# Kernel tuning notes

Measured on AMD Instinct MI355X. Metric: run time of the kernel, lower is better.

The kernel has to match this reference:

```python
import jax, jax.numpy as jnp
import numpy as np

DIM = 1024
DEPTH = 2
D_STATE = 16
EXPAND = 2            # standard Mamba expand factor -> d_inner = 2*dim
D_CONV = 4
DT_RANK = DIM // 16   # ceil(dim/16) = 64
D_INNER = DIM * EXPAND
BATCH = 2
SEQ = 1024


def setup_inputs() -> dict:
    key = jax.random.key(0)
    ks = jax.random.split(key, 8)
    def n(k, shape, scale):
        return jax.random.normal(k, shape, jnp.float32) * scale
    # A_log initialized as log(1..N) per channel (S4D-real init, as in mamba_ssm)
    A_log = jnp.tile(jnp.log(jnp.arange(1, D_STATE + 1, dtype=jnp.float32))[None, None, :],
                     (DEPTH, D_INNER, 1))
    return {
        "x": n(ks[0], (BATCH, SEQ, DIM), 1.0),
        "in_proj_w": n(ks[1], (DEPTH, 2 * D_INNER, DIM), DIM ** -0.5),
        "conv_w": n(ks[2], (DEPTH, D_INNER, D_CONV), D_CONV ** -0.5),
        "conv_b": jnp.zeros((DEPTH, D_INNER), jnp.float32),
        "x_proj_w": n(ks[3], (DEPTH, DT_RANK + 2 * D_STATE, D_INNER), D_INNER ** -0.5),
        "dt_proj_w": n(ks[4], (DEPTH, D_INNER, DT_RANK), DT_RANK ** -0.5),
        "dt_proj_b": n(ks[5], (DEPTH, D_INNER), 0.1),
        "A_log": A_log,
        "D": jnp.ones((DEPTH, D_INNER), jnp.float32),
        "out_proj_w": n(ks[6], (DEPTH, DIM, D_INNER), D_INNER ** -0.5),
    }


def _mamba_layer(x, in_w, cw, cb, xp_w, dtw, dtb, A_log, Dp, ow):
    # x: [B, L, dim]
    Bsz = x.shape[0]
    xz = jnp.einsum('bld,ed->ble', x, in_w)            # [B, L, 2*d_inner]
    xi, z = jnp.split(xz, 2, axis=-1)
    # causal depthwise conv1d over time
    xc = jnp.transpose(xi, (0, 2, 1))                  # [B, d_inner, L]
    xc = jax.lax.conv_general_dilated(xc, cw[:, None, :], (1,), [(D_CONV - 1, 0)],
                                      feature_group_count=D_INNER)
    xc = xc + cb[None, :, None]
    xc = jax.nn.silu(jnp.transpose(xc, (0, 2, 1)))     # [B, L, d_inner]
    # input-dependent dt, B, C
    x_dbl = jnp.einsum('bld,ed->ble', xc, xp_w)        # [B, L, dt_rank+2*N]
    dt_raw = x_dbl[..., :DT_RANK]
    Bm = x_dbl[..., DT_RANK:DT_RANK + D_STATE]         # [B, L, N]
    Cm = x_dbl[..., DT_RANK + D_STATE:]                # [B, L, N]
    dt = jax.nn.softplus(jnp.einsum('blr,dr->bld', dt_raw, dtw) + dtb)  # [B, L, d_inner]
    A = -jnp.exp(A_log)                                # [d_inner, N]
    dA = jnp.exp(dt[..., None] * A[None, None])        # [B, L, d_inner, N]
    dBu = dt[..., None] * Bm[:, :, None, :] * xc[..., None]

    def step(h, inp):
        dA_t, dBu_t, C_t = inp
        h = dA_t * h + dBu_t                           # [B, d_inner, N]
        y = jnp.einsum('bdn,bn->bd', h, C_t)
        return h, y

    h0 = jnp.zeros((Bsz, D_INNER, D_STATE), x.dtype)
    _, ys = jax.lax.scan(step, h0,
                         (dA.transpose(1, 0, 2, 3), dBu.transpose(1, 0, 2, 3),
                          Cm.transpose(1, 0, 2)))
    y = ys.transpose(1, 0, 2) + Dp[None, None, :] * xc
    y = y * jax.nn.silu(z)
    return jnp.einsum('bld,od->blo', y, ow)


def reference(x, in_proj_w, conv_w, conv_b, x_proj_w, dt_proj_w, dt_proj_b, A_log, D, out_proj_w):
    for i in range(DEPTH):
        x = _mamba_layer(x, in_proj_w[i], conv_w[i], conv_b[i], x_proj_w[i],
                         dt_proj_w[i], dt_proj_b[i], A_log[i], D[i], out_proj_w[i])
    return x
```

## Files before the change

### kernel.cpp

```cpp
#include <hip/hip_runtime.h>
#include <hip/hip_bf16.h>

typedef __hip_bfloat16 bf16;
typedef __attribute__((ext_vector_type(8))) short short8;
typedef __attribute__((ext_vector_type(4))) short shortx4;
typedef __attribute__((ext_vector_type(4))) float floatx4;

#define BATCH   2
#define SEQ     1024
#define DIM     1024
#define D_INNER 2048
#define D_STATE 16
#define DT_RANK 64
#define MROWS   (BATCH * SEQ)
#define CHUNK   32
#define NCHUNK  (SEQ / CHUNK)

__device__ __forceinline__ float bf2f(bf16 x) { return __bfloat162float(x); }
__device__ __forceinline__ bf16  f2bf(float x) { return __float2bfloat16(x); }
__device__ __forceinline__ short bfbits(float x) {
    bf16 b = __float2bfloat16(x); short s; __builtin_memcpy(&s, &b, 2); return s;
}

__device__ __forceinline__ void ld_lds16(const void* g, void* l) {
    __builtin_amdgcn_global_load_lds(
        (const __attribute__((address_space(1))) void*)g,
        (__attribute__((address_space(3))) void*)l, 16, 0, 0);
}

__device__ __forceinline__ void cast4(const float* in, short* o, int i) {
    floatx4 v = ((const floatx4*)in)[i];
    shortx4 r;
    r.x = bfbits(v.x); r.y = bfbits(v.y); r.z = bfbits(v.z); r.w = bfbits(v.w);
    ((shortx4*)o)[i] = r;
}
__global__ __launch_bounds__(256) void cast_k(
    const float* __restrict__ in, short* __restrict__ o, int n4)
{
    int i = blockIdx.x * 256 + threadIdx.x;
    if (i < n4) cast4(in, o, i);
}
__global__ __launch_bounds__(256) void cast2_k(
    const float* __restrict__ a, short* __restrict__ oa, int na4,
    const float* __restrict__ b, short* __restrict__ ob, int nb4)
{
    int i = blockIdx.x * 256 + threadIdx.x;
    if (i < na4) cast4(a, oa, i);
    else if (i - na4 < nb4) cast4(b, ob, i - na4);
}

__device__ __forceinline__ short8 ld8_any(const void* p, size_t eoff, int is_f32) {
    if (is_f32) {
        const float* f = (const float*)p + eoff;
        floatx4 a = *(const floatx4*)f;
        floatx4 b = *(const floatx4*)(f + 4);
        short8 r;
        r[0] = bfbits(a[0]); r[1] = bfbits(a[1]); r[2] = bfbits(a[2]); r[3] = bfbits(a[3]);
        r[4] = bfbits(b[0]); r[5] = bfbits(b[1]); r[6] = bfbits(b[2]); r[7] = bfbits(b[3]);
        return r;
    } else {
        return *(const short8*)((const bf16*)p + eoff);
    }
}

__global__ __launch_bounds__(256) void gemm128(
    const bf16* __restrict__ A, int lda,
    const bf16* __restrict__ B, int ldb,
    float* __restrict__ Cf, bf16* __restrict__ Cb, int ldc,
    int kchunk, size_t psize)
{
    __shared__ short As[4][128 * 32];
    __shared__ short Bs[4][128 * 32];
    const int tid  = threadIdx.x;
    const int wave = tid >> 6;
    const int lane = tid & 63;
    const int m0 = blockIdx.y * 128;
    const int n0 = blockIdx.x * 128;
    const int wm = (wave & 1) * 64;
    const int wn = (wave >> 1) * 64;
    const int r16  = lane & 15;
    const int quad = lane >> 4;
    const int r0   = tid >> 2;
    const int csw   = (((tid & 3) ^ ((r0 >> 1) & 3)) << 3);
    const int swoff = ((quad ^ ((r16 >> 1) & 3)) << 3);
    const int kbeg = blockIdx.z * kchunk;
    const int nk   = kchunk >> 5;

    floatx4 acc[4][4] = {};

    auto STAGE = [&](int buf, int kk) {
        ld_lds16(A + (size_t)(m0 + r0) * lda + kk + csw,      &As[buf][tid * 8]);
        ld_lds16(A + (size_t)(m0 + r0 + 64) * lda + kk + csw, &As[buf][(tid + 256) * 8]);
        ld_lds16(B + (size_t)(n0 + r0) * ldb + kk + csw,      &Bs[buf][tid * 8]);
        ld_lds16(B + (size_t)(n0 + r0 + 64) * ldb + kk + csw, &Bs[buf][(tid + 256) * 8]);
    };
    auto COMPUTE = [&](int buf) {
        const short* Ab = As[buf];
        const short* Bb = Bs[buf];
        short8 af[4], bg[4];
#pragma unroll
        for (int i = 0; i < 4; i++) {
            af[i] = *(const short8*)(Ab + (wm + i * 16 + r16) * 32 + swoff);
            bg[i] = *(const short8*)(Bb + (wn + i * 16 + r16) * 32 + swoff);
        }
        __builtin_amdgcn_s_setprio(1);
#pragma unroll
        for (int i = 0; i < 4; i++)
#pragma unroll
            for (int j = 0; j < 4; j++)
                acc[i][j] = __builtin_amdgcn_mfma_f32_16x16x32_bf16(af[i], bg[j], acc[i][j], 0, 0, 0);
        __builtin_amdgcn_s_setprio(0);
    };

    STAGE(0, kbeg);
    STAGE(1, kbeg + 32);
    int it = 0;
    for (; it < nk - 2; ++it) {
        STAGE((it + 2) & 3, kbeg + (it + 2) * 32);
        asm volatile("s_waitcnt vmcnt(8) lgkmcnt(0)" ::: "memory");
        __builtin_amdgcn_s_barrier();
        __builtin_amdgcn_sched_barrier(0);
        COMPUTE(it & 3);
    }
    asm volatile("s_waitcnt vmcnt(4) lgkmcnt(0)" ::: "memory");
    __builtin_amdgcn_s_barrier();
    __builtin_amdgcn_sched_barrier(0);
    COMPUTE(it & 3);
    ++it;
    asm volatile("s_waitcnt vmcnt(0) lgkmcnt(0)" ::: "memory");
    __builtin_amdgcn_s_barrier();
    __builtin_amdgcn_sched_barrier(0);
    COMPUTE(it & 3);

    float* Cfp = Cf ? Cf + (size_t)blockIdx.z * psize : nullptr;
#pragma unroll
    for (int i = 0; i < 4; i++)
#pragma unroll
        for (int j = 0; j < 4; j++) {
            int gm = m0 + wm + i * 16 + quad * 4;
            int gn = n0 + wn + j * 16 + r16;
#pragma unroll
            for (int r = 0; r < 4; r++) {
                size_t o = (size_t)(gm + r) * ldc + gn;
                float v = acc[i][j][r];
                if (Cfp) Cfp[o] = v;
                if (Cb) Cb[o] = f2bf(v);
            }
        }
}

__global__ __launch_bounds__(256) void gemm_bt(
    const void* __restrict__ A, int a_f32, int lda,
    const void* __restrict__ B, int b_f32, int ldb,
    float* __restrict__ Cf, bf16* __restrict__ Cb, int ldc,
    int N, int K, size_t psize,
    const float* __restrict__ bias, int act)
{
    __shared__ short As[64][40];
    __shared__ short Bs[64][40];
    const int m0   = blockIdx.y * 64;
    const int n0   = blockIdx.x * 64;
    const int tid  = threadIdx.x;
    const int wave = tid >> 6;
    const int lane = tid & 63;
    const int srow = tid >> 2;
    const int scol = (tid & 3) << 3;
    const int r16  = lane & 15;
    const int quad = lane >> 4;
    const int kbeg = blockIdx.z * K;

    floatx4 acc[4] = {};

    for (int k0 = kbeg; k0 < kbeg + K; k0 += 32) {
        short8 av = ld8_any(A, (size_t)(m0 + srow) * lda + k0 + scol, a_f32);
        short8 bv = {};
        int gn = n0 + srow;
        if (gn < N) bv = ld8_any(B, (size_t)gn * ldb + k0 + scol, b_f32);
        *(short8*)(&As[srow][scol]) = av;
        *(short8*)(&Bs[srow][scol]) = bv;
        __syncthreads();
        short8 af = *(const short8*)(&As[wave * 16 + r16][quad * 8]);
#pragma unroll
        for (int nt = 0; nt < 4; nt++) {
            short8 bq = *(const short8*)(&Bs[nt * 16 + r16][quad * 8]);
            acc[nt] = __builtin_amdgcn_mfma_f32_16x16x32_bf16(af, bq, acc[nt], 0, 0, 0);
        }
        __syncthreads();
    }

    float* Cfp = Cf ? Cf + (size_t)blockIdx.z * psize : nullptr;
#pragma unroll
    for (int nt = 0; nt < 4; nt++) {
        int gn = n0 + nt * 16 + r16;
        if (gn >= N) continue;
        float bsv = bias ? bias[gn] : 0.f;
#pragma unroll
        for (int r = 0; r < 4; r++) {
            int gm = m0 + wave * 16 + quad * 4 + r;
            float v = acc[nt][r] + bsv;
            if (act == 1) v = (v > 20.f) ? v : log1pf(__expf(v));
            size_t o = (size_t)gm * ldc + gn;
            if (Cfp) Cfp[o] = v;
            if (Cb) Cb[o] = f2bf(v);
        }
    }
}

__global__ __launch_bounds__(256) void reduceN_k(
    const float* __restrict__ part, size_t psize, int n, int np,
    float* __restrict__ of, bf16* __restrict__ ob)
{
    int i = blockIdx.x * 256 + threadIdx.x;
    if (i >= n) return;
    float v = 0.f;
    for (int j = 0; j < np; j++) v += part[i + (size_t)j * psize];
    if (of) of[i] = v;
    if (ob) ob[i] = f2bf(v);
}

__global__ __launch_bounds__(256) void conv_silu_k(
    const bf16* __restrict__ xz, const float* __restrict__ cw,
    const float* __restrict__ cb, bf16* __restrict__ xcb)
{
    int idx = blockIdx.x * 256 + threadIdx.x;
    int d   = idx & (D_INNER - 1);
    int bt  = idx >> 11;
    int t   = bt & (SEQ - 1);
    float s = cb[d];
#pragma unroll
    for (int j = 0; j < 4; j++) {
        int tt = t - 3 + j;
        if (tt >= 0) s += cw[d * 4 + j] * bf2f(xz[(size_t)(bt - 3 + j) * 4096 + d]);
    }
    float sig = 1.f / (1.f + __expf(-s));
    xcb[idx] = f2bf(s * sig);
}

__global__ __launch_bounds__(256) void scan1_k(
    const float* __restrict__ dtf, const bf16* __restrict__ xcb,
    const float* __restrict__ xdbl, const float* __restrict__ Alog,
    float* __restrict__ chunk_sdt, float* __restrict__ chunk_S)
{
    __shared__ float dt_s[CHUNK][256];
    __shared__ short xc_s[CHUNK][256];
    __shared__ float B_s[CHUNK][16];
    const int tid = threadIdx.x;
    const int d0  = blockIdx.x * 256;
    const int d   = d0 + tid;
    const int b   = blockIdx.y;
    const int c   = blockIdx.z;
    const size_t rbase = (size_t)b * SEQ + c * CHUNK;

#pragma unroll 4
    for (int t = 0; t < CHUNK; t++) {
        dt_s[t][tid] = dtf[(rbase + t) * D_INNER + d0 + tid];
        ((short*)xc_s)[t * 256 + tid] = *(const short*)&xcb[(rbase + t) * D_INNER + d0 + tid];
    }
    for (int e = tid; e < CHUNK * 16; e += 256) {
        int t = e >> 4, n = e & 15;
        B_s[t][n] = xdbl[(rbase + t) * 96 + 64 + n];
    }
    float A[16];
#pragma unroll
    for (int n = 0; n < 16; n++) A[n] = -__expf(Alog[(size_t)d * 16 + n]);
    float h[16] = {};
    float sdt = 0.f;
    __syncthreads();

    for (int t = 0; t < CHUNK; t++) {
        float dtv = dt_s[t][tid];
        bf16 xcr; short xs = xc_s[t][tid]; __builtin_memcpy(&xcr, &xs, 2);
        float u = dtv * bf2f(xcr);
        sdt += dtv;
        floatx4 B0 = *(const floatx4*)&B_s[t][0];
        floatx4 B1 = *(const floatx4*)&B_s[t][4];
        floatx4 B2 = *(const floatx4*)&B_s[t][8];
        floatx4 B3 = *(const floatx4*)&B_s[t][12];
#pragma unroll
        for (int n = 0; n < 4; n++) {
            h[n]      = __expf(dtv * A[n])      * h[n]      + u * B0[n];
            h[n + 4]  = __expf(dtv * A[n + 4])  * h[n + 4]  + u * B1[n];
            h[n + 8]  = __expf(dtv * A[n + 8])  * h[n + 8]  + u * B2[n];
            h[n + 12] = __expf(dtv * A[n + 12]) * h[n + 12] + u * B3[n];
        }
    }
    chunk_sdt[(b * NCHUNK + c) * D_INNER + d] = sdt;
#pragma unroll
    for (int n = 0; n < 16; n++)
        chunk_S[((size_t)(b * NCHUNK + c) * 16 + n) * D_INNER + d] = h[n];
}

__global__ __launch_bounds__(256) void scanpre_k(
    const float* __restrict__ Alog, const float* __restrict__ chunk_sdt,
    float* __restrict__ chunk_S)
{
    const int d = blockIdx.x * 256 + threadIdx.x;
    const int b = blockIdx.y;
    const int n = blockIdx.z;
    const float Av = -__expf(Alog[(size_t)d * 16 + n]);
    float h = 0.f;
    for (int j = 0; j < NCHUNK; j++) {
        size_t si = ((size_t)(b * NCHUNK + j) * 16 + n) * D_INNER + d;
        float S   = chunk_S[si];
        float sdt = chunk_sdt[(b * NCHUNK + j) * D_INNER + d];
        chunk_S[si] = h;
        h = __expf(sdt * Av) * h + S;
    }
}

__global__ __launch_bounds__(256) void scan2_k(
    const float* __restrict__ dtf, const bf16* __restrict__ xcb,
    const float* __restrict__ xdbl, const bf16* __restrict__ xz,
    const float* __restrict__ Alog, const float* __restrict__ Dp,
    const float* __restrict__ chunk_S, bf16* __restrict__ yb)
{
    __shared__ float dt_s[CHUNK][256];
    __shared__ short xc_s[CHUNK][256];
    __shared__ float B_s[CHUNK][16];
    __shared__ float C_s[CHUNK][16];
    const int tid = threadIdx.x;
    const int d0  = blockIdx.x * 256;
    const int d   = d0 + tid;
    const int b   = blockIdx.y;
    const int c   = blockIdx.z;
    const size_t rbase = (size_t)b * SEQ + c * CHUNK;

#pragma unroll 4
    for (int t = 0; t < CHUNK; t++) {
        dt_s[t][tid] = dtf[(rbase + t) * D_INNER + d0 + tid];
        ((short*)xc_s)[t * 256 + tid] = *(const short*)&xcb[(rbase + t) * D_INNER + d0 + tid];
    }
    for (int e = tid; e < CHUNK * 16; e += 256) {
        int t = e >> 4, n = e & 15;
        B_s[t][n] = xdbl[(rbase + t) * 96 + 64 + n];
        C_s[t][n] = xdbl[(rbase + t) * 96 + 80 + n];
    }
    float A[16];
#pragma unroll
    for (int n = 0; n < 16; n++) A[n] = -__expf(Alog[(size_t)d * 16 + n]);

    float h[16];
#pragma unroll
    for (int n = 0; n < 16; n++)
        h[n] = chunk_S[((size_t)(b * NCHUNK + c) * 16 + n) * D_INNER + d];

    const float Dv = Dp[d];
    __syncthreads();

    for (int t = 0; t < CHUNK; t++) {
        size_t row = rbase + t;
        float dtv = dt_s[t][tid];
        bf16 xcr; short xs = xc_s[t][tid]; __builtin_memcpy(&xcr, &xs, 2);
        float xcv = bf2f(xcr);
        float u = dtv * xcv;
        floatx4 B0 = *(const floatx4*)&B_s[t][0];
        floatx4 B1 = *(const floatx4*)&B_s[t][4];
        floatx4 B2 = *(const floatx4*)&B_s[t][8];
        floatx4 B3 = *(const floatx4*)&B_s[t][12];
        floatx4 C0 = *(const floatx4*)&C_s[t][0];
        floatx4 C1 = *(const floatx4*)&C_s[t][4];
        floatx4 C2 = *(const floatx4*)&C_s[t][8];
        floatx4 C3 = *(const floatx4*)&C_s[t][12];
        float y = 0.f;
#pragma unroll
        for (int n = 0; n < 4; n++) {
            h[n]      = __expf(dtv * A[n])      * h[n]      + u * B0[n];
            h[n + 4]  = __expf(dtv * A[n + 4])  * h[n + 4]  + u * B1[n];
            h[n + 8]  = __expf(dtv * A[n + 8])  * h[n + 8]  + u * B2[n];
            h[n + 12] = __expf(dtv * A[n + 12]) * h[n + 12] + u * B3[n];
            y += h[n] * C0[n] + h[n + 4] * C1[n] + h[n + 8] * C2[n] + h[n + 12] * C3[n];
        }
        float zv = bf2f(xz[row * 4096 + 2048 + d]);
        y = (y + Dv * xcv) * (zv / (1.f + __expf(-zv)));
        yb[row * D_INNER + d] = f2bf(y);
    }
}

extern "C" void kernel_launch(void* const* d_in, const int* in_sizes, int n_in,
                              void* d_out, int out_size, void* d_ws, size_t ws_size,
                              hipStream_t stream)
{
    const float* x    = (const float*)d_in[0];
    const float* inw  = (const float*)d_in[1];
    const float* cw   = (const float*)d_in[2];
    const float* cb   = (const float*)d_in[3];
    const float* xpw  = (const float*)d_in[4];
    const float* dtw  = (const float*)d_in[5];
    const float* dtb  = (const float*)d_in[6];
    const float* Alog = (const float*)d_in[7];
    const float* Dp   = (const float*)d_in[8];
    const float* ow   = (const float*)d_in[9];
    float* out = (float*)d_out;

    char* p = (char*)d_ws;
    bf16*  xzb   = (bf16*)p;  p += (size_t)MROWS * 4096 * 2;
    bf16*  xcb   = (bf16*)p;  p += (size_t)MROWS * D_INNER * 2;
    float* xdblf = (float*)p; p += (size_t)MROWS * 96 * 4;
    float* dtf   = (float*)p; p += (size_t)MROWS * D_INNER * 4;
    bf16*  ybf   = (bf16*)p;  p += (size_t)MROWS * D_INNER * 2;
    bf16*  xmid  = (bf16*)p;  p += (size_t)MROWS * DIM * 2;
    float* csdt  = (float*)p; p += (size_t)BATCH * NCHUNK * D_INNER * 4;
    float* cS    = (float*)p; p += (size_t)BATCH * NCHUNK * 16 * D_INNER * 4;
    bf16*  xb    = (bf16*)p;  p += (size_t)MROWS * DIM * 2;
    bf16*  inwb  = (bf16*)p;  p += (size_t)2 * D_INNER * DIM * 2;
    bf16*  owb   = (bf16*)p;  p += (size_t)DIM * D_INNER * 2;
    float* xprt  = (float*)p; p += (size_t)8 * MROWS * 96 * 4;
    float* oprt  = (float*)p; p += (size_t)4 * MROWS * DIM * 4;

    const size_t xp_psize = (size_t)MROWS * 96;
    const size_t op_psize = (size_t)MROWS * DIM;

    cast_k<<<(MROWS * DIM / 4 + 255) / 256, 256, 0, stream>>>(x, (short*)xb, MROWS * DIM / 4);

    for (int l = 0; l < 2; l++) {
        const float* xpw_l = xpw + (size_t)l * 96 * D_INNER;
        const float* dtw_l = dtw + (size_t)l * D_INNER * DT_RANK;
        const float* Al    = Alog + (size_t)l * D_INNER * D_STATE;

        {
            int na4 = 2 * D_INNER * DIM / 4, nb4 = DIM * D_INNER / 4;
            cast2_k<<<(na4 + nb4 + 255) / 256, 256, 0, stream>>>(
                inw + (size_t)l * 2 * D_INNER * DIM, (short*)inwb, na4,
                ow + (size_t)l * DIM * D_INNER, (short*)owb, nb4);
        }

        gemm128<<<dim3(32, 16, 1), 256, 0, stream>>>(
            (l == 0) ? xb : xmid, DIM, inwb, DIM,
            nullptr, xzb, 4096, DIM, 0);

        conv_silu_k<<<(MROWS * D_INNER) / 256, 256, 0, stream>>>(
            xzb, cw + (size_t)l * D_INNER * 4, cb + (size_t)l * D_INNER, xcb);

        gemm_bt<<<dim3(2, 32, 8), 256, 0, stream>>>(
            xcb, 0, D_INNER, xpw_l, 1, D_INNER,
            xprt, nullptr, 96, 96, 256, xp_psize, nullptr, 0);
        reduceN_k<<<(MROWS * 96 + 255) / 256, 256, 0, stream>>>(
            xprt, xp_psize, MROWS * 96, 8, xdblf, nullptr);

        gemm_bt<<<dim3(32, 32), 256, 0, stream>>>(
            xdblf, 1, 96, dtw_l, 1, DT_RANK,
            dtf, nullptr, D_INNER, D_INNER, DT_RANK, 0,
            dtb + (size_t)l * D_INNER, 1);

        scan1_k<<<dim3(D_INNER / 256, BATCH, NCHUNK), 256, 0, stream>>>(
            dtf, xcb, xdblf, Al, csdt, cS);
        scanpre_k<<<dim3(D_INNER / 256, BATCH, D_STATE), 256, 0, stream>>>(
            Al, csdt, cS);
        scan2_k<<<dim3(D_INNER / 256, BATCH, NCHUNK), 256, 0, stream>>>(
            dtf, xcb, xdblf, xzb, Al, Dp + (size_t)l * D_INNER, cS, ybf);

        gemm128<<<dim3(8, 16, 4), 256, 0, stream>>>(
            ybf, D_INNER, owb, D_INNER,
            oprt, nullptr, DIM, D_INNER / 4, op_psize);
        reduceN_k<<<(MROWS * DIM + 255) / 256, 256, 0, stream>>>(
            oprt, op_psize, MROWS * DIM, 4,
            (l == 1) ? out : nullptr, (l == 0) ? xmid : nullptr);
    }
}
```

Baseline: 422.7 us.

## Fuse chunked scan passes into one cooperative kernel; vectorize conv+silu

The three scan kernels (chunk-local state, cross-chunk prefix, output pass) are merged into one cooperative kernel that uses grid-wide syncs between the phases. dt, xc and B stay in shared memory across phases, so they are no longer reloaded from global memory, and two kernel launches are removed. The conv+SiLU kernel now has each thread handle 8 channels with vector loads and stores. The cooperative launch requires all 512 blocks to be co-resident, and the grid syncs add their own cost. Only 2*8*16 blocks do the serial prefix while the rest wait at the sync.

```diff
diff --git a/kernel.cpp b/kernel.cpp
--- a/kernel.cpp
+++ b/kernel.cpp
@@ -1,5 +1,8 @@
 #include <hip/hip_runtime.h>
 #include <hip/hip_bf16.h>
+#include <hip/hip_cooperative_groups.h>
+
+namespace cg = cooperative_groups;
 
 typedef __hip_bfloat16 bf16;
 typedef __attribute__((ext_vector_type(8))) short short8;
@@ -20,6 +23,9 @@
 __device__ __forceinline__ bf16  f2bf(float x) { return __float2bfloat16(x); }
 __device__ __forceinline__ short bfbits(float x) {
     bf16 b = __float2bfloat16(x); short s; __builtin_memcpy(&s, &b, 2); return s;
+}
+__device__ __forceinline__ float bits2f(short s) {
+    bf16 b; __builtin_memcpy(&b, &s, 2); return __bfloat162float(b);
 }
 
 __device__ __forceinline__ void ld_lds16(const void* g, void* l) {
@@ -223,96 +229,44 @@
     const float* __restrict__ cb, bf16* __restrict__ xcb)
 {
     int idx = blockIdx.x * 256 + threadIdx.x;
-    int d   = idx & (D_INNER - 1);
-    int bt  = idx >> 11;
+    int d   = (idx & 255) << 3;
+    int bt  = idx >> 8;
     int t   = bt & (SEQ - 1);
-    float s = cb[d];
+
+    float s[8];
+    floatx4 cb0 = *(const floatx4*)(cb + d);
+    floatx4 cb1 = *(const floatx4*)(cb + d + 4);
+#pragma unroll
+    for (int i = 0; i < 4; i++) { s[i] = cb0[i]; s[i + 4] = cb1[i]; }
+
+    floatx4 w[8];
+#pragma unroll
+    for (int i = 0; i < 8; i++) w[i] = *(const floatx4*)(cw + (d + i) * 4);
+
 #pragma unroll
     for (int j = 0; j < 4; j++) {
         int tt = t - 3 + j;
-        if (tt >= 0) s += cw[d * 4 + j] * bf2f(xz[(size_t)(bt - 3 + j) * 4096 + d]);
-    }
-    float sig = 1.f / (1.f + __expf(-s));
-    xcb[idx] = f2bf(s * sig);
-}
-
-__global__ __launch_bounds__(256) void scan1_k(
-    const float* __restrict__ dtf, const bf16* __restrict__ xcb,
-    const float* __restrict__ xdbl, const float* __restrict__ Alog,
-    float* __restrict__ chunk_sdt, float* __restrict__ chunk_S)
-{
-    __shared__ float dt_s[CHUNK][256];
-    __shared__ short xc_s[CHUNK][256];
-    __shared__ float B_s[CHUNK][16];
-    const int tid = threadIdx.x;
-    const int d0  = blockIdx.x * 256;
-    const int d   = d0 + tid;
-    const int b   = blockIdx.y;
-    const int c   = blockIdx.z;
-    const size_t rbase = (size_t)b * SEQ + c * CHUNK;
-
-#pragma unroll 4
-    for (int t = 0; t < CHUNK; t++) {
-        dt_s[t][tid] = dtf[(rbase + t) * D_INNER + d0 + tid];
-        ((short*)xc_s)[t * 256 + tid] = *(const short*)&xcb[(rbase + t) * D_INNER + d0 + tid];
-    }
-    for (int e = tid; e < CHUNK * 16; e += 256) {
-        int t = e >> 4, n = e & 15;
-        B_s[t][n] = xdbl[(rbase + t) * 96 + 64 + n];
-    }
-    float A[16];
-#pragma unroll
-    for (int n = 0; n < 16; n++) A[n] = -__expf(Alog[(size_t)d * 16 + n]);
-    float h[16] = {};
-    float sdt = 0.f;
-    __syncthreads();
-
-    for (int t = 0; t < CHUNK; t++) {
-        float dtv = dt_s[t][tid];
-        bf16 xcr; short xs = xc_s[t][tid]; __builtin_memcpy(&xcr, &xs, 2);
-        float u = dtv * bf2f(xcr);
-        sdt += dtv;
-        floatx4 B0 = *(const floatx4*)&B_s[t][0];
-        floatx4 B1 = *(const floatx4*)&B_s[t][4];
-        floatx4 B2 = *(const floatx4*)&B_s[t][8];
-        floatx4 B3 = *(const floatx4*)&B_s[t][12];
-#pragma unroll
-        for (int n = 0; n < 4; n++) {
-            h[n]      = __expf(dtv * A[n])      * h[n]      + u * B0[n];
-            h[n + 4]  = __expf(dtv * A[n + 4])  * h[n + 4]  + u * B1[n];
-            h[n + 8]  = __expf(dtv * A[n + 8])  * h[n + 8]  + u * B2[n];
-            h[n + 12] = __expf(dtv * A[n + 12]) * h[n + 12] + u * B3[n];
-        }
-    }
-    chunk_sdt[(b * NCHUNK + c) * D_INNER + d] = sdt;
-#pragma unroll
-    for (int n = 0; n < 16; n++)
-        chunk_S[((size_t)(b * NCHUNK + c) * 16 + n) * D_INNER + d] = h[n];
-}
-
-__global__ __launch_bounds__(256) void scanpre_k(
-    const float* __restrict__ Alog, const float* __restrict__ chunk_sdt,
-    float* __restrict__ chunk_S)
-{
-    const int d = blockIdx.x * 256 + threadIdx.x;
-    const int b = blockIdx.y;
-    const int n = blockIdx.z;
-    const float Av = -__expf(Alog[(size_t)d * 16 + n]);
-    float h = 0.f;
-    for (int j = 0; j < NCHUNK; j++) {
-        size_t si = ((size_t)(b * NCHUNK + j) * 16 + n) * D_INNER + d;
-        float S   = chunk_S[si];
-        float sdt = chunk_sdt[(b * NCHUNK + j) * D_INNER + d];
-        chunk_S[si] = h;
-        h = __expf(sdt * Av) * h + S;
-    }
-}
-
-__global__ __launch_bounds__(256) void scan2_k(
+        if (tt >= 0) {
+            short8 v = *(const short8*)&xz[(size_t)(bt - 3 + j) * 4096 + d];
+#pragma unroll
+            for (int i = 0; i < 8; i++) s[i] += w[i][j] * bits2f(v[i]);
+        }
+    }
+    short8 r;
+#pragma unroll
+    for (int i = 0; i < 8; i++) {
+        float sig = 1.f / (1.f + __expf(-s[i]));
+        r[i] = bfbits(s[i] * sig);
+    }
+    *(short8*)&xcb[(size_t)bt * D_INNER + d] = r;
+}
+
+__global__ __launch_bounds__(256) void scan_fused_k(
     const float* __restrict__ dtf, const bf16* __restrict__ xcb,
     const float* __restrict__ xdbl, const bf16* __restrict__ xz,
     const float* __restrict__ Alog, const float* __restrict__ Dp,
-    const float* __restrict__ chunk_S, bf16* __restrict__ yb)
+    float* __restrict__ chunk_sdt, float* __restrict__ chunk_S,
+    bf16* __restrict__ yb)
 {
     __shared__ float dt_s[CHUNK][256];
     __shared__ short xc_s[CHUNK][256];
@@ -338,20 +292,59 @@
     float A[16];
 #pragma unroll
     for (int n = 0; n < 16; n++) A[n] = -__expf(Alog[(size_t)d * 16 + n]);
-
-    float h[16];
+    float h[16] = {};
+    float sdt = 0.f;
+    __syncthreads();
+
+    for (int t = 0; t < CHUNK; t++) {
+        float dtv = dt_s[t][tid];
+        float u = dtv * bits2f(xc_s[t][tid]);
+        sdt += dtv;
+        floatx4 B0 = *(const floatx4*)&B_s[t][0];
+        floatx4 B1 = *(const floatx4*)&B_s[t][4];
+        floatx4 B2 = *(const floatx4*)&B_s[t][8];
+        floatx4 B3 = *(const floatx4*)&B_s[t][12];
+#pragma unroll
+        for (int n = 0; n < 4; n++) {
+            h[n]      = __expf(dtv * A[n])      * h[n]      + u * B0[n];
+            h[n + 4]  = __expf(dtv * A[n + 4])  * h[n + 4]  + u * B1[n];
+            h[n + 8]  = __expf(dtv * A[n + 8])  * h[n + 8]  + u * B2[n];
+            h[n + 12] = __expf(dtv * A[n + 12]) * h[n + 12] + u * B3[n];
+        }
+    }
+    chunk_sdt[(b * NCHUNK + c) * D_INNER + d] = sdt;
+#pragma unroll
+    for (int n = 0; n < 16; n++)
+        chunk_S[((size_t)(b * NCHUNK + c) * 16 + n) * D_INNER + d] = h[n];
+
+    __threadfence();
+    cg::this_grid().sync();
+
+    if (c < D_STATE) {
+        const int n = c;
+        const float Av = -__expf(Alog[(size_t)d * 16 + n]);
+        float hp = 0.f;
+        for (int j = 0; j < NCHUNK; j++) {
+            size_t si = ((size_t)(b * NCHUNK + j) * 16 + n) * D_INNER + d;
+            float S   = chunk_S[si];
+            float sj  = chunk_sdt[(b * NCHUNK + j) * D_INNER + d];
+            chunk_S[si] = hp;
+            hp = __expf(sj * Av) * hp + S;
+        }
+    }
+
+    __threadfence();
+    cg::this_grid().sync();
+
 #pragma unroll
     for (int n = 0; n < 16; n++)
         h[n] = chunk_S[((size_t)(b * NCHUNK + c) * 16 + n) * D_INNER + d];
-
     const float Dv = Dp[d];
-    __syncthreads();
 
     for (int t = 0; t < CHUNK; t++) {
         size_t row = rbase + t;
         float dtv = dt_s[t][tid];
-        bf16 xcr; short xs = xc_s[t][tid]; __builtin_memcpy(&xcr, &xs, 2);
-        float xcv = bf2f(xcr);
+        float xcv = bits2f(xc_s[t][tid]);
         float u = dtv * xcv;
         floatx4 B0 = *(const floatx4*)&B_s[t][0];
         floatx4 B1 = *(const floatx4*)&B_s[t][4];
@@ -416,6 +409,7 @@
         const float* xpw_l = xpw + (size_t)l * 96 * D_INNER;
         const float* dtw_l = dtw + (size_t)l * D_INNER * DT_RANK;
         const float* Al    = Alog + (size_t)l * D_INNER * D_STATE;
+        const float* Dl    = Dp + (size_t)l * D_INNER;
 
         {
             int na4 = 2 * D_INNER * DIM / 4, nb4 = DIM * D_INNER / 4;
@@ -428,7 +422,7 @@
             (l == 0) ? xb : xmid, DIM, inwb, DIM,
             nullptr, xzb, 4096, DIM, 0);
 
-        conv_silu_k<<<(MROWS * D_INNER) / 256, 256, 0, stream>>>(
+        conv_silu_k<<<(MROWS * D_INNER / 8) / 256, 256, 0, stream>>>(
             xzb, cw + (size_t)l * D_INNER * 4, cb + (size_t)l * D_INNER, xcb);
 
         gemm_bt<<<dim3(2, 32, 8), 256, 0, stream>>>(
@@ -442,12 +436,14 @@
             dtf, nullptr, D_INNER, D_INNER, DT_RANK, 0,
             dtb + (size_t)l * D_INNER, 1);
 
-        scan1_k<<<dim3(D_INNER / 256, BATCH, NCHUNK), 256, 0, stream>>>(
-            dtf, xcb, xdblf, Al, csdt, cS);
-        scanpre_k<<<dim3(D_INNER / 256, BATCH, D_STATE), 256, 0, stream>>>(
-            Al, csdt, cS);
-        scan2_k<<<dim3(D_INNER / 256, BATCH, NCHUNK), 256, 0, stream>>>(
-            dtf, xcb, xdblf, xzb, Al, Dp + (size_t)l * D_INNER, cS, ybf);
+        {
+            void* args[] = {
+                (void*)&dtf, (void*)&xcb, (void*)&xdblf, (void*)&xzb,
+                (void*)&Al, (void*)&Dl, (void*)&csdt, (void*)&cS, (void*)&ybf
+            };
+            hipLaunchCooperativeKernel((void*)scan_fused_k,
+                dim3(D_INNER / 256, BATCH, NCHUNK), dim3(256), args, 0, stream);
+        }
 
         gemm128<<<dim3(8, 16, 4), 256, 0, stream>>>(
             ybf, D_INNER, owb, D_INNER,
```

Measured after the change: 809.4 us. +91.5%, slower.
